# Optimization experiments

Measured on AMD Instinct MI355X. Metric: run time of the kernel, lower is better.

Reference implementation:

```python
import jax, jax.numpy as jnp
import numpy as np

C_Z = 128
H = 4
D = C_Z // H          # head_dim = 32
BASE = 2 * D // 2     # base_feature_dim = feature_map_multiplier*head_dim//2 = 32
BSZ, S = 1, 256
EPS_LN = 1e-5


def _lin_params(key, fan_in, fan_out):
    kw, kb = jax.random.split(key)
    bound = 1.0 / np.sqrt(fan_in)
    w = jax.random.uniform(kw, (fan_out, fan_in), jnp.float32, -bound, bound)
    b = jax.random.uniform(kb, (fan_out,), jnp.float32, -bound, bound)
    return w, b


def setup_inputs() -> dict:
    key = jax.random.key(0)
    ks = jax.random.split(key, 9)
    z = jax.random.normal(ks[0], (BSZ, S, S, C_Z), jnp.float32)
    pair_mask = jax.random.randint(ks[1], (BSZ, S, S), 0, 2, jnp.int32)
    q_w, q_b = _lin_params(ks[2], C_Z, C_Z)
    k_w, k_b = _lin_params(ks[3], C_Z, C_Z)
    v_w, v_b = _lin_params(ks[4], C_Z, C_Z)
    qf_w, qf_b = _lin_params(ks[5], D, BASE)
    kf_w, kf_b = _lin_params(ks[6], D, BASE)
    g_w, g_b = _lin_params(ks[7], C_Z, C_Z)
    o_w, o_b = _lin_params(ks[8], C_Z, C_Z)
    return {
        'z': z, 'pair_mask': pair_mask,
        'ln_w': jnp.ones((C_Z,), jnp.float32), 'ln_b': jnp.zeros((C_Z,), jnp.float32),
        'q_w': q_w, 'q_b': q_b, 'k_w': k_w, 'k_b': k_b, 'v_w': v_w, 'v_b': v_b,
        'qf_w': qf_w, 'qf_b': qf_b, 'kf_w': kf_w, 'kf_b': kf_b,
        'g_w': g_w, 'g_b': g_b, 'o_w': o_w, 'o_b': o_b,
    }


def _feature_map(t, w, b):
    m = jnp.clip(t @ w.T + b, -8.0, 8.0)
    return jnp.concatenate([jnp.exp(m), jnp.exp(-m)], axis=-1)


def reference(z, pair_mask, ln_w, ln_b, q_w, q_b, k_w, k_b, v_w, v_b,
              qf_w, qf_b, kf_w, kf_b, g_w, g_b, o_w, o_b):
    bsz, seq, _, c = z.shape
    h, d = H, c // H
    mask = pair_mask.astype(z.dtype)                         # [B,S,S]

    # LayerNorm over last dim
    mu = jnp.mean(z, axis=-1, keepdims=True)
    var = jnp.mean(jnp.square(z - mu), axis=-1, keepdims=True)
    zn = (z - mu) * jax.lax.rsqrt(var + EPS_LN) * ln_w + ln_b

    z_rows = zn.reshape(bsz * seq, seq, c)                   # [BS, N, C]
    row_mask = mask.reshape(bsz * seq, seq)[:, None, :, None]  # [BS,1,N,1]

    def proj(w, b):
        return (z_rows @ w.T + b).reshape(bsz * seq, seq, h, d).transpose(0, 2, 1, 3)

    q = proj(q_w, q_b)                                       # [BS,H,N,D]
    k = proj(k_w, k_b)
    v = proj(v_w, v_b) * row_mask

    qf = _feature_map(q, qf_w, qf_b)                         # [BS,H,N,F]
    kf = _feature_map(k, kf_w, kf_b) * row_mask

    kv = jnp.einsum('bhnd,bhne->bhde', kf, v)                # [BS,H,F,D]
    k_sum = kf.sum(axis=-2)                                  # [BS,H,F]
    denom = jnp.maximum(jnp.einsum('bhnd,bhd->bhn', qf, k_sum), 1e-6)
    out = jnp.einsum('bhnd,bhde->bhne', qf, kv) / denom[..., None]

    out = out.transpose(0, 2, 1, 3).reshape(bsz * seq, seq, c)
    gate = jax.nn.sigmoid(z_rows @ g_w.T + g_b)
    out = (gate * out) @ o_w.T + o_b
    out = out.reshape(bsz, seq, seq, c)
    return out * mask[..., None]
```

## Files before the change

### kernel.cpp

```cpp
#include <hip/hip_runtime.h>
#include <stdint.h>

#define DEV __device__ __forceinline__

typedef unsigned short u16;
typedef unsigned int u32;
typedef short bh8 __attribute__((ext_vector_type(8)));
typedef float f32x4 __attribute__((ext_vector_type(4)));

DEV float bf2f(u16 v){ return __uint_as_float(((u32)v)<<16); }
DEV u16 f2bf(float f){
    u32 x = __float_as_uint(f);
    x += 0x7fffu + ((x>>16)&1u);
    return (u16)(x>>16);
}
DEV void cvt8(int4 r, float* f){
    u32 a=(u32)r.x, b=(u32)r.y, c=(u32)r.z, d=(u32)r.w;
    f[0]=__uint_as_float(a<<16); f[1]=__uint_as_float(a&0xffff0000u);
    f[2]=__uint_as_float(b<<16); f[3]=__uint_as_float(b&0xffff0000u);
    f[4]=__uint_as_float(c<<16); f[5]=__uint_as_float(c&0xffff0000u);
    f[6]=__uint_as_float(d<<16); f[7]=__uint_as_float(d&0xffff0000u);
}
DEV int2 pk4(float a, float b, float c, float d){
    int2 r;
    r.x = (int)((u32)f2bf(a) | ((u32)f2bf(b)<<16));
    r.y = (int)((u32)f2bf(c) | ((u32)f2bf(d)<<16));
    return r;
}
DEV bh8 ld_frag(const u16* p){
    int4 v = *(const int4*)p;
    union{ int4 i; bh8 h; } u; u.i = v; return u.h;
}
#define MFMA __builtin_amdgcn_mfma_f32_16x16x32_bf16


#define P_LNW 0
#define P_LNB 128
#define P_QW  256
#define P_QB  16640
#define P_KW  16768
#define P_KB  33152
#define P_VW  33280
#define P_VB  49664
#define P_QFW 49792
#define P_QFB 50816
#define P_KFW 50848
#define P_KFB 51872
#define P_GW  51904
#define P_GB  68288
#define P_OW  68416
#define P_OB  84800
#define P_TOT 84928
#define P_CQW 84928
#define P_CQB 101312
#define P_CKW 101440
#define P_CKB 117824

#define NCONV 332

__global__ void prep_params(
    const float* p0, const float* p1, const float* p2, const float* p3,
    const float* p4, const float* p5, const float* p6, const float* p7,
    const float* p8, const float* p9, const float* p10, const float* p11,
    const float* p12, const float* p13, const float* p14, const float* p15,
    u16* __restrict__ dst){
    int b = blockIdx.x, tid = threadIdx.x;
    if(b < NCONV){
        int idx = b*256 + tid;
        if(idx >= P_TOT) return;
        const int offs[17] = {P_LNW,P_LNB,P_QW,P_QB,P_KW,P_KB,P_VW,P_VB,
                              P_QFW,P_QFB,P_KFW,P_KFB,P_GW,P_GB,P_OW,P_OB,P_TOT};
        const float* ptrs[16] = {p0,p1,p2,p3,p4,p5,p6,p7,p8,p9,p10,p11,p12,p13,p14,p15};
        int tsel = 0;
        #pragma unroll
        for(int i=1;i<16;++i) if(idx >= offs[i]) tsel = i;
        dst[idx] = f2bf(ptrs[tsel][idx - offs[tsel]]);
    } else if(b < NCONV + 128){
        int idx = (b - NCONV)*256 + tid;
        int sel = idx >> 14;
        int rem = idx & 16383;
        int h = rem >> 12, j = (rem >> 7) & 31, c = rem & 127;
        const float* FWp = sel ? p10 : p8;
        const float* Wp  = sel ? p4  : p2;
        float s = 0.f;
        #pragma unroll
        for(int d=0; d<32; ++d)
            s += FWp[j*32+d] * Wp[(h*32+d)*128 + c];
        dst[(sel ? P_CKW : P_CQW) + h*4096 + j*128 + c] = f2bf(s);
    } else {
        int t = tid;
        int sel = t >> 7, h = (t >> 5) & 3, j = t & 31;
        const float* FWp = sel ? p10 : p8;
        const float* FBp = sel ? p11 : p9;
        const float* Bp  = sel ? p5  : p3;
        float s = FBp[j];
        #pragma unroll
        for(int d=0; d<32; ++d)
            s += FWp[j*32+d] * Bp[h*32+d];
        dst[(sel ? P_CKB : P_CQB) + h*32 + j] = f2bf(s);
    }
}

__global__ void ln_kernel(const float* __restrict__ zv, const u16* __restrict__ pb,
                          u16* __restrict__ zn){
    int t = blockIdx.x*4 + (threadIdx.x>>6);
    int lane = threadIdx.x & 63;
    float2 v = ((const float2*)zv)[(size_t)t*64 + lane];
    float x0 = v.x, x1 = v.y;
    float s = x0 + x1, s2 = x0*x0 + x1*x1;
    #pragma unroll
    for(int o=1;o<64;o<<=1){ s += __shfl_xor(s,o,64); s2 += __shfl_xor(s2,o,64); }
    float mean = s*(1.f/128.f);
    float var  = s2*(1.f/128.f) - mean*mean;
    float rs = rsqrtf(var + 1e-5f);
    int c0 = 2*lane;
    float w0 = bf2f(pb[P_LNW+c0]), w1 = bf2f(pb[P_LNW+c0+1]);
    float b0 = bf2f(pb[P_LNB+c0]), b1 = bf2f(pb[P_LNB+c0+1]);
    float o0 = (x0-mean)*rs*w0 + b0;
    float o1 = (x1-mean)*rs*w1 + b1;
    u32 po = (u32)f2bf(o0) | ((u32)f2bf(o1)<<16);
    *(u32*)(zn + (size_t)t*128 + c0) = po;
}

#define ST_N 260
#define ST_F 68
#define KVT_OFF 22712
#define LDS_U16 (96*ST_N)

__global__ __launch_bounds__(256,2)
void mega_kernel(const u16* __restrict__ zn, const int* __restrict__ mask,
                 const u16* __restrict__ pb, u16* __restrict__ attn){
    __shared__ __align__(16) u16 lds[LDS_U16];
    u16* kfT = lds;
    u16* vT  = lds + 64*ST_N;
    u16* qf  = lds;
    u16* kvT = lds + KVT_OFF;

    int g = blockIdx.x, row = g>>2, h = g&3;
    int tid = threadIdx.x, lane = tid & 63, wv = tid >> 6;
    int lm = lane & 15, quad = lane >> 4;

    u32 mbits = 0;
    {
        const int4* mp = (const int4*)(mask + row*256 + wv*64 + quad*4);
        #pragma unroll
        for(int mt=0; mt<4; ++mt){
            int4 m = mp[mt*4];
            mbits |= ((u32)(m.x&1))<<(4*mt) | ((u32)(m.y&1))<<(4*mt+1)
                   | ((u32)(m.z&1))<<(4*mt+2) | ((u32)(m.w&1))<<(4*mt+3);
        }
    }

    bh8 a[4][4];
    {
        const u16* Ab = zn + ((size_t)row*256 + wv*64 + lm)*128 + quad*8;
        #pragma unroll
        for(int mt=0; mt<4; ++mt)
            #pragma unroll
            for(int ks=0; ks<4; ++ks)
                a[mt][ks] = ld_frag(Ab + (size_t)mt*16*128 + ks*32);
    }
    bh8 onesf;
    { union{int4 i; bh8 h;} u2; u2.i.x=u2.i.y=u2.i.z=u2.i.w=0x3F803F80; onesf = u2.h; }

    f32x4 gacc[4][2];
    {
        f32x4 acc[4][6];
        #pragma unroll
        for(int mt=0;mt<4;++mt)
            #pragma unroll
            for(int j=0;j<6;++j) acc[mt][j] = (f32x4){0,0,0,0};
        #pragma unroll
        for(int ks=0; ks<4; ++ks){
            bh8 b[6];
            b[0] = ld_frag(pb + P_CKW + h*4096 + lm*128            + ks*32 + quad*8);
            b[1] = ld_frag(pb + P_CKW + h*4096 + (16+lm)*128       + ks*32 + quad*8);
            b[2] = ld_frag(pb + P_VW + (size_t)(h*32 + lm)*128     + ks*32 + quad*8);
            b[3] = ld_frag(pb + P_VW + (size_t)(h*32 + 16+lm)*128  + ks*32 + quad*8);
            b[4] = ld_frag(pb + P_GW + (size_t)(h*32 + lm)*128     + ks*32 + quad*8);
            b[5] = ld_frag(pb + P_GW + (size_t)(h*32 + 16+lm)*128  + ks*32 + quad*8);
            #pragma unroll
            for(int mt=0; mt<4; ++mt)
                #pragma unroll
                for(int j=0;j<6;++j)
                    acc[mt][j] = MFMA(a[mt][ks], b[j], acc[mt][j], 0,0,0);
        }
        float bk0 = bf2f(pb[P_CKB + h*32 + lm]);
        float bk1 = bf2f(pb[P_CKB + h*32 + 16 + lm]);
        float bv0 = bf2f(pb[P_VB + h*32 + lm]);
        float bv1 = bf2f(pb[P_VB + h*32 + 16 + lm]);
        float bg0 = bf2f(pb[P_GB + h*32 + lm]);
        float bg1 = bf2f(pb[P_GB + h*32 + 16 + lm]);
        #pragma unroll
        for(int mt=0; mt<4; ++mt){
            int n0 = wv*64 + mt*16 + quad*4;
            float ep0[4], em0[4], ep1[4], em1[4], v0[4], v1[4];
            #pragma unroll
            for(int r=0; r<4; ++r){
                float mk = (float)((mbits>>(4*mt+r))&1u);
                float m0 = fminf(8.f, fmaxf(-8.f, acc[mt][0][r] + bk0));
                float m1 = fminf(8.f, fmaxf(-8.f, acc[mt][1][r] + bk1));
                ep0[r] = __expf( m0)*mk;  em0[r] = __expf(-m0)*mk;
                ep1[r] = __expf( m1)*mk;  em1[r] = __expf(-m1)*mk;
                v0[r] = (acc[mt][2][r] + bv0)*mk;
                v1[r] = (acc[mt][3][r] + bv1)*mk;
                gacc[mt][0][r] = 1.f/(1.f + __expf(-(acc[mt][4][r] + bg0)));
                gacc[mt][1][r] = 1.f/(1.f + __expf(-(acc[mt][5][r] + bg1)));
            }
            *(int2*)(kfT + (size_t)(4*lm  )*ST_N + n0) = pk4(ep0[0],ep0[1],ep0[2],ep0[3]);
            *(int2*)(kfT + (size_t)(4*lm+1)*ST_N + n0) = pk4(em0[0],em0[1],em0[2],em0[3]);
            *(int2*)(kfT + (size_t)(4*lm+2)*ST_N + n0) = pk4(ep1[0],ep1[1],ep1[2],ep1[3]);
            *(int2*)(kfT + (size_t)(4*lm+3)*ST_N + n0) = pk4(em1[0],em1[1],em1[2],em1[3]);
            *(int2*)(vT  + (size_t)(lm   )*ST_N + n0) = pk4(v0[0],v0[1],v0[2],v0[3]);
            *(int2*)(vT  + (size_t)(16+lm)*ST_N + n0) = pk4(v1[0],v1[1],v1[2],v1[3]);
        }
    }
    __syncthreads();
    f32x4 kv0=(f32x4){0,0,0,0}, kv1=(f32x4){0,0,0,0}, ksm=(f32x4){0,0,0,0};
    #pragma unroll
    for(int ks=0; ks<8; ++ks){
        bh8 aa = ld_frag(kfT + (size_t)(wv*16+lm)*ST_N + ks*32 + quad*8);
        bh8 b0 = ld_frag(vT + (size_t)lm*ST_N      + ks*32 + quad*8);
        bh8 b1 = ld_frag(vT + (size_t)(16+lm)*ST_N + ks*32 + quad*8);
        kv0 = MFMA(aa, b0, kv0, 0,0,0);
        kv1 = MFMA(aa, b1, kv1, 0,0,0);
        ksm = MFMA(aa, onesf, ksm, 0,0,0);
    }
    __syncthreads();
    {
        int f0 = wv*16 + quad*4;
        *(int2*)(kvT + (size_t)(lm   )*ST_F + f0) = pk4(kv0[0],kv0[1],kv0[2],kv0[3]);
        *(int2*)(kvT + (size_t)(16+lm)*ST_F + f0) = pk4(kv1[0],kv1[1],kv1[2],kv1[3]);
        if(lm==0)
            *(int2*)(kvT + (size_t)32*ST_F + f0) = pk4(ksm[0],ksm[1],ksm[2],ksm[3]);
    }
    {
        f32x4 acc[4][2];
        #pragma unroll
        for(int mt=0;mt<4;++mt){ acc[mt][0]=(f32x4){0,0,0,0}; acc[mt][1]=(f32x4){0,0,0,0}; }
        #pragma unroll
        for(int ks=0; ks<4; ++ks){
            bh8 b0 = ld_frag(pb + P_CQW + h*4096 + lm*128      + ks*32 + quad*8);
            bh8 b1 = ld_frag(pb + P_CQW + h*4096 + (16+lm)*128 + ks*32 + quad*8);
            #pragma unroll
            for(int mt=0; mt<4; ++mt){
                acc[mt][0] = MFMA(a[mt][ks], b0, acc[mt][0], 0,0,0);
                acc[mt][1] = MFMA(a[mt][ks], b1, acc[mt][1], 0,0,0);
            }
        }
        float bb0 = bf2f(pb[P_CQB + h*32 + lm]);
        float bb1 = bf2f(pb[P_CQB + h*32 + 16 + lm]);
        #pragma unroll
        for(int mt=0; mt<4; ++mt)
            #pragma unroll
            for(int r=0; r<4; ++r){
                int n = wv*64 + mt*16 + quad*4 + r;
                float m0 = fminf(8.f, fmaxf(-8.f, acc[mt][0][r] + bb0));
                float m1 = fminf(8.f, fmaxf(-8.f, acc[mt][1][r] + bb1));
                *(int2*)(qf + (size_t)n*ST_F + 4*lm) =
                    pk4(__expf(m0), __expf(-m0), __expf(m1), __expf(-m1));
            }
    }
    __syncthreads();
    {
        f32x4 acc[4][3];
        #pragma unroll
        for(int mt=0;mt<4;++mt)
            #pragma unroll
            for(int nt=0;nt<3;++nt) acc[mt][nt]=(f32x4){0,0,0,0};
        #pragma unroll
        for(int ks=0; ks<2; ++ks){
            bh8 b0 = ld_frag(kvT + (size_t)lm*ST_F      + ks*32 + quad*8);
            bh8 b1 = ld_frag(kvT + (size_t)(16+lm)*ST_F + ks*32 + quad*8);
            bh8 b2 = ld_frag(kvT + (size_t)32*ST_F      + ks*32 + quad*8);
            #pragma unroll
            for(int mt=0; mt<4; ++mt){
                bh8 aa = ld_frag(qf + (size_t)(wv*64+mt*16+lm)*ST_F + ks*32 + quad*8);
                acc[mt][0] = MFMA(aa, b0, acc[mt][0], 0,0,0);
                acc[mt][1] = MFMA(aa, b1, acc[mt][1], 0,0,0);
                acc[mt][2] = MFMA(aa, b2, acc[mt][2], 0,0,0);
            }
        }
        #pragma unroll
        for(int mt=0; mt<4; ++mt)
            #pragma unroll
            for(int r=0; r<4; ++r){
                int n = wv*64 + mt*16 + quad*4 + r;
                float rcp = 1.f / fmaxf(acc[mt][2][r], 1e-6f);
                u16* op = attn + ((size_t)row*256 + n)*128 + h*32;
                op[lm]    = f2bf(acc[mt][0][r]*rcp*gacc[mt][0][r]);
                op[16+lm] = f2bf(acc[mt][1][r]*rcp*gacc[mt][1][r]);
            }
    }
}

#define LDS_P 136
__global__ __launch_bounds__(256,2)
void oproj_kernel(const u16* __restrict__ attn, const u16* __restrict__ pb,
                  const int* __restrict__ mask, float* __restrict__ out){
    __shared__ u16 st[128*LDS_P];
    int tid = threadIdx.x;
    int lane = tid&63, wv = tid>>6;
    int mhalf = (wv>>1)*64, nhalf = (wv&1)*64;
    int lm = lane&15, quad = lane>>4;
    int m0 = blockIdx.x*128;

    f32x4 acc[4][4];
    #pragma unroll
    for(int mt=0;mt<4;++mt)
        #pragma unroll
        for(int nt=0;nt<4;++nt)
            acc[mt][nt] = (f32x4){0.f,0.f,0.f,0.f};

    const u16* Abase = attn + (size_t)(m0 + mhalf + lm)*128 + quad*8;
    const u16* W = pb + P_OW;
    #pragma unroll
    for(int ks=0; ks<4; ++ks){
        bh8 a[4], b[4];
        #pragma unroll
        for(int mt=0; mt<4; ++mt)
            a[mt] = ld_frag(Abase + (size_t)mt*16*128 + ks*32);
        #pragma unroll
        for(int nt=0; nt<4; ++nt)
            b[nt] = ld_frag(W + (size_t)(nhalf + nt*16 + lm)*128 + ks*32 + quad*8);
        #pragma unroll
        for(int mt=0; mt<4; ++mt)
            #pragma unroll
            for(int nt=0; nt<4; ++nt)
                acc[mt][nt] = MFMA(a[mt], b[nt], acc[mt][nt], 0, 0, 0);
    }
    float bv[4];
    #pragma unroll
    for(int nt=0; nt<4; ++nt) bv[nt] = bf2f(pb[P_OB + nhalf + nt*16 + lm]);
    #pragma unroll
    for(int mt=0; mt<4; ++mt){
        int mrow = m0 + mhalf + mt*16 + quad*4;
        float mk[4];
        #pragma unroll
        for(int r=0;r<4;++r) mk[r] = (float)mask[mrow+r];
        #pragma unroll
        for(int nt=0; nt<4; ++nt)
            #pragma unroll
            for(int r=0; r<4; ++r){
                float x = (acc[mt][nt][r] + bv[nt]) * mk[r];
                st[(mhalf + mt*16 + quad*4 + r)*LDS_P + nhalf + nt*16 + lm] = f2bf(x);
            }
    }
    __syncthreads();
    {
        int row = tid>>1, half = tid&1;
        const u16* src = st + row*LDS_P + half*64;
        float* dst = out + (size_t)(m0 + row)*128 + half*64;
        #pragma unroll
        for(int it=0; it<8; ++it){
            float f[8]; cvt8(((const int4*)src)[it], f);
            float4 lo; lo.x=f[0]; lo.y=f[1]; lo.z=f[2]; lo.w=f[3];
            float4 hi; hi.x=f[4]; hi.y=f[5]; hi.z=f[6]; hi.w=f[7];
            ((float4*)dst)[it*2  ] = lo;
            ((float4*)dst)[it*2+1] = hi;
        }
    }
}

extern "C" void kernel_launch(void* const* d_in, const int* in_sizes, int n_in,
                              void* d_out, int out_size, void* d_ws, size_t ws_size,
                              hipStream_t stream){
    const float* z    = (const float*)d_in[0];
    const int*   mask = (const int*)d_in[1];

    char* ws = (char*)d_ws;
    const size_t MB = (size_t)1<<20;
    u16* zn   = (u16*)(ws + 0*MB);
    u16* attn = (u16*)(ws + 16*MB);
    u16* pb   = (u16*)(ws + 32*MB);

    prep_params<<<NCONV+129,256,0,stream>>>(
        (const float*)d_in[2],  (const float*)d_in[3],  (const float*)d_in[4],  (const float*)d_in[5],
        (const float*)d_in[6],  (const float*)d_in[7],  (const float*)d_in[8],  (const float*)d_in[9],
        (const float*)d_in[10], (const float*)d_in[11], (const float*)d_in[12], (const float*)d_in[13],
        (const float*)d_in[14], (const float*)d_in[15], (const float*)d_in[16], (const float*)d_in[17],
        pb);
    ln_kernel<<<16384,256,0,stream>>>(z, pb, zn);
    mega_kernel<<<1024,256,0,stream>>>(zn, mask, pb, attn);
    oproj_kernel<<<512,256,0,stream>>>(attn, pb, mask, (float*)d_out);
}
```

Before: 187.2 us.

## Reload zn fragments per half-tile to cut registers and raise occupancy to 3

```diff
diff --git a/kernel.cpp b/kernel.cpp
--- a/kernel.cpp
+++ b/kernel.cpp
@@ -127,7 +127,7 @@
 #define KVT_OFF 22712
 #define LDS_U16 (96*ST_N)
 
-__global__ __launch_bounds__(256,2)
+__global__ __launch_bounds__(256,3)
 void mega_kernel(const u16* __restrict__ zn, const int* __restrict__ mask,
                  const u16* __restrict__ pb, u16* __restrict__ attn){
     __shared__ __align__(16) u16 lds[LDS_U16];
@@ -151,68 +151,65 @@
         }
     }
 
-    bh8 a[4][4];
-    {
-        const u16* Ab = zn + ((size_t)row*256 + wv*64 + lm)*128 + quad*8;
-        #pragma unroll
-        for(int mt=0; mt<4; ++mt)
-            #pragma unroll
-            for(int ks=0; ks<4; ++ks)
-                a[mt][ks] = ld_frag(Ab + (size_t)mt*16*128 + ks*32);
-    }
     bh8 onesf;
     { union{int4 i; bh8 h;} u2; u2.i.x=u2.i.y=u2.i.z=u2.i.w=0x3F803F80; onesf = u2.h; }
 
-    f32x4 gacc[4][2];
-    {
-        f32x4 acc[4][6];
-        #pragma unroll
-        for(int mt=0;mt<4;++mt)
-            #pragma unroll
-            for(int j=0;j<6;++j) acc[mt][j] = (f32x4){0,0,0,0};
-        #pragma unroll
-        for(int ks=0; ks<4; ++ks){
-            bh8 b[6];
-            b[0] = ld_frag(pb + P_CKW + h*4096 + lm*128            + ks*32 + quad*8);
-            b[1] = ld_frag(pb + P_CKW + h*4096 + (16+lm)*128       + ks*32 + quad*8);
-            b[2] = ld_frag(pb + P_VW + (size_t)(h*32 + lm)*128     + ks*32 + quad*8);
-            b[3] = ld_frag(pb + P_VW + (size_t)(h*32 + 16+lm)*128  + ks*32 + quad*8);
-            b[4] = ld_frag(pb + P_GW + (size_t)(h*32 + lm)*128     + ks*32 + quad*8);
-            b[5] = ld_frag(pb + P_GW + (size_t)(h*32 + 16+lm)*128  + ks*32 + quad*8);
-            #pragma unroll
-            for(int mt=0; mt<4; ++mt)
-                #pragma unroll
-                for(int j=0;j<6;++j)
-                    acc[mt][j] = MFMA(a[mt][ks], b[j], acc[mt][j], 0,0,0);
-        }
+    const u16* Abase = zn + ((size_t)row*256 + wv*64 + lm)*128 + quad*8;
+
+    {
         float bk0 = bf2f(pb[P_CKB + h*32 + lm]);
         float bk1 = bf2f(pb[P_CKB + h*32 + 16 + lm]);
         float bv0 = bf2f(pb[P_VB + h*32 + lm]);
         float bv1 = bf2f(pb[P_VB + h*32 + 16 + lm]);
-        float bg0 = bf2f(pb[P_GB + h*32 + lm]);
-        float bg1 = bf2f(pb[P_GB + h*32 + 16 + lm]);
-        #pragma unroll
-        for(int mt=0; mt<4; ++mt){
-            int n0 = wv*64 + mt*16 + quad*4;
-            float ep0[4], em0[4], ep1[4], em1[4], v0[4], v1[4];
-            #pragma unroll
-            for(int r=0; r<4; ++r){
-                float mk = (float)((mbits>>(4*mt+r))&1u);
-                float m0 = fminf(8.f, fmaxf(-8.f, acc[mt][0][r] + bk0));
-                float m1 = fminf(8.f, fmaxf(-8.f, acc[mt][1][r] + bk1));
-                ep0[r] = __expf( m0)*mk;  em0[r] = __expf(-m0)*mk;
-                ep1[r] = __expf( m1)*mk;  em1[r] = __expf(-m1)*mk;
-                v0[r] = (acc[mt][2][r] + bv0)*mk;
-                v1[r] = (acc[mt][3][r] + bv1)*mk;
-                gacc[mt][0][r] = 1.f/(1.f + __expf(-(acc[mt][4][r] + bg0)));
-                gacc[mt][1][r] = 1.f/(1.f + __expf(-(acc[mt][5][r] + bg1)));
-            }
-            *(int2*)(kfT + (size_t)(4*lm  )*ST_N + n0) = pk4(ep0[0],ep0[1],ep0[2],ep0[3]);
-            *(int2*)(kfT + (size_t)(4*lm+1)*ST_N + n0) = pk4(em0[0],em0[1],em0[2],em0[3]);
-            *(int2*)(kfT + (size_t)(4*lm+2)*ST_N + n0) = pk4(ep1[0],ep1[1],ep1[2],ep1[3]);
-            *(int2*)(kfT + (size_t)(4*lm+3)*ST_N + n0) = pk4(em1[0],em1[1],em1[2],em1[3]);
-            *(int2*)(vT  + (size_t)(lm   )*ST_N + n0) = pk4(v0[0],v0[1],v0[2],v0[3]);
-            *(int2*)(vT  + (size_t)(16+lm)*ST_N + n0) = pk4(v1[0],v1[1],v1[2],v1[3]);
+        #pragma unroll 1
+        for(int hm=0; hm<2; ++hm){
+            bh8 a2[2][4];
+            const u16* Ab = Abase + (size_t)hm*32*128;
+            #pragma unroll
+            for(int m=0; m<2; ++m)
+                #pragma unroll
+                for(int ks=0; ks<4; ++ks)
+                    a2[m][ks] = ld_frag(Ab + (size_t)m*16*128 + ks*32);
+            f32x4 acc[2][4];
+            #pragma unroll
+            for(int m=0;m<2;++m)
+                #pragma unroll
+                for(int j=0;j<4;++j) acc[m][j] = (f32x4){0,0,0,0};
+            #pragma unroll
+            for(int ks=0; ks<4; ++ks){
+                bh8 b[4];
+                b[0] = ld_frag(pb + P_CKW + h*4096 + lm*128            + ks*32 + quad*8);
+                b[1] = ld_frag(pb + P_CKW + h*4096 + (16+lm)*128       + ks*32 + quad*8);
+                b[2] = ld_frag(pb + P_VW + (size_t)(h*32 + lm)*128     + ks*32 + quad*8);
+                b[3] = ld_frag(pb + P_VW + (size_t)(h*32 + 16+lm)*128  + ks*32 + quad*8);
+                #pragma unroll
+                for(int m=0; m<2; ++m)
+                    #pragma unroll
+                    for(int j=0;j<4;++j)
+                        acc[m][j] = MFMA(a2[m][ks], b[j], acc[m][j], 0,0,0);
+            }
+            #pragma unroll
+            for(int m=0; m<2; ++m){
+                int mt = hm*2 + m;
+                int n0 = wv*64 + mt*16 + quad*4;
+                float ep0[4], em0[4], ep1[4], em1[4], v0[4], v1[4];
+                #pragma unroll
+                for(int r=0; r<4; ++r){
+                    float mk = (float)((mbits>>(4*mt+r))&1u);
+                    float m0 = fminf(8.f, fmaxf(-8.f, acc[m][0][r] + bk0));
+                    float m1 = fminf(8.f, fmaxf(-8.f, acc[m][1][r] + bk1));
+                    ep0[r] = __expf( m0)*mk;  em0[r] = __expf(-m0)*mk;
+                    ep1[r] = __expf( m1)*mk;  em1[r] = __expf(-m1)*mk;
+                    v0[r] = (acc[m][2][r] + bv0)*mk;
+                    v1[r] = (acc[m][3][r] + bv1)*mk;
+                }
+                *(int2*)(kfT + (size_t)(4*lm  )*ST_N + n0) = pk4(ep0[0],ep0[1],ep0[2],ep0[3]);
+                *(int2*)(kfT + (size_t)(4*lm+1)*ST_N + n0) = pk4(em0[0],em0[1],em0[2],em0[3]);
+                *(int2*)(kfT + (size_t)(4*lm+2)*ST_N + n0) = pk4(ep1[0],ep1[1],ep1[2],ep1[3]);
+                *(int2*)(kfT + (size_t)(4*lm+3)*ST_N + n0) = pk4(em1[0],em1[1],em1[2],em1[3]);
+                *(int2*)(vT  + (size_t)(lm   )*ST_N + n0) = pk4(v0[0],v0[1],v0[2],v0[3]);
+                *(int2*)(vT  + (size_t)(16+lm)*ST_N + n0) = pk4(v1[0],v1[1],v1[2],v1[3]);
+            }
         }
     }
     __syncthreads();
@@ -234,32 +231,54 @@
         if(lm==0)
             *(int2*)(kvT + (size_t)32*ST_F + f0) = pk4(ksm[0],ksm[1],ksm[2],ksm[3]);
     }
-    {
-        f32x4 acc[4][2];
-        #pragma unroll
-        for(int mt=0;mt<4;++mt){ acc[mt][0]=(f32x4){0,0,0,0}; acc[mt][1]=(f32x4){0,0,0,0}; }
-        #pragma unroll
-        for(int ks=0; ks<4; ++ks){
-            bh8 b0 = ld_frag(pb + P_CQW + h*4096 + lm*128      + ks*32 + quad*8);
-            bh8 b1 = ld_frag(pb + P_CQW + h*4096 + (16+lm)*128 + ks*32 + quad*8);
-            #pragma unroll
-            for(int mt=0; mt<4; ++mt){
-                acc[mt][0] = MFMA(a[mt][ks], b0, acc[mt][0], 0,0,0);
-                acc[mt][1] = MFMA(a[mt][ks], b1, acc[mt][1], 0,0,0);
-            }
-        }
+    f32x4 gacc[4][2];
+    {
         float bb0 = bf2f(pb[P_CQB + h*32 + lm]);
         float bb1 = bf2f(pb[P_CQB + h*32 + 16 + lm]);
-        #pragma unroll
-        for(int mt=0; mt<4; ++mt)
-            #pragma unroll
-            for(int r=0; r<4; ++r){
-                int n = wv*64 + mt*16 + quad*4 + r;
-                float m0 = fminf(8.f, fmaxf(-8.f, acc[mt][0][r] + bb0));
-                float m1 = fminf(8.f, fmaxf(-8.f, acc[mt][1][r] + bb1));
-                *(int2*)(qf + (size_t)n*ST_F + 4*lm) =
-                    pk4(__expf(m0), __expf(-m0), __expf(m1), __expf(-m1));
-            }
+        float bg0 = bf2f(pb[P_GB + h*32 + lm]);
+        float bg1 = bf2f(pb[P_GB + h*32 + 16 + lm]);
+        #pragma unroll
+        for(int hm=0; hm<2; ++hm){
+            bh8 a2[2][4];
+            const u16* Ab = Abase + (size_t)hm*32*128;
+            #pragma unroll
+            for(int m=0; m<2; ++m)
+                #pragma unroll
+                for(int ks=0; ks<4; ++ks)
+                    a2[m][ks] = ld_frag(Ab + (size_t)m*16*128 + ks*32);
+            f32x4 acc[2][4];
+            #pragma unroll
+            for(int m=0;m<2;++m)
+                #pragma unroll
+                for(int j=0;j<4;++j) acc[m][j] = (f32x4){0,0,0,0};
+            #pragma unroll
+            for(int ks=0; ks<4; ++ks){
+                bh8 b[4];
+                b[0] = ld_frag(pb + P_CQW + h*4096 + lm*128            + ks*32 + quad*8);
+                b[1] = ld_frag(pb + P_CQW + h*4096 + (16+lm)*128       + ks*32 + quad*8);
+                b[2] = ld_frag(pb + P_GW + (size_t)(h*32 + lm)*128     + ks*32 + quad*8);
+                b[3] = ld_frag(pb + P_GW + (size_t)(h*32 + 16+lm)*128  + ks*32 + quad*8);
+                #pragma unroll
+                for(int m=0; m<2; ++m)
+                    #pragma unroll
+                    for(int j=0;j<4;++j)
+                        acc[m][j] = MFMA(a2[m][ks], b[j], acc[m][j], 0,0,0);
+            }
+            #pragma unroll
+            for(int m=0; m<2; ++m){
+                const int mt = hm*2 + m;
+                #pragma unroll
+                for(int r=0; r<4; ++r){
+                    int n = wv*64 + mt*16 + quad*4 + r;
+                    float m0 = fminf(8.f, fmaxf(-8.f, acc[m][0][r] + bb0));
+                    float m1 = fminf(8.f, fmaxf(-8.f, acc[m][1][r] + bb1));
+                    *(int2*)(qf + (size_t)n*ST_F + 4*lm) =
+                        pk4(__expf(m0), __expf(-m0), __expf(m1), __expf(-m1));
+                    gacc[mt][0][r] = 1.f/(1.f + __expf(-(acc[m][2][r] + bg0)));
+                    gacc[mt][1][r] = 1.f/(1.f + __expf(-(acc[m][3][r] + bg1)));
+                }
+            }
+        }
     }
     __syncthreads();
     {
```

Result: slower. 196.0 us (+4.7%).
